# Kernel optimization log

Measured on AMD Instinct MI355X. Metric: run time of the kernel, lower is better.

The kernel has to match this reference:

```python
import jax, jax.numpy as jnp
import numpy as np

B, N, F_IN = 256, 256, 128
HID, DEPTH = 48, 4
D_OUT = 97                 # sum(latent_dim [32,32,32,1]) = GraphUNet out_channels
K_SORT = 30
C1, C2, KW2 = 16, 32, 5
POOL_LEN = (K_SORT - 2) // 2 + 1        # 15 after maxpool1d(2,2)
DENSE_DIM = (POOL_LEN - KW2 + 1) * C2   # 352
OUT_DIM = 32


def _gcn(x, A, W, b):
    # GCNConv(improved=True): A_hat = A + 2I; out = D^-1/2 A_hat D^-1/2 (x W) + b
    n = A.shape[-1]
    Ah = A + 2.0 * jnp.eye(n, dtype=A.dtype)
    dinv = jax.lax.rsqrt(jnp.sum(Ah, axis=-1))          # deg >= 2 always
    An = dinv[:, :, None] * Ah * dinv[:, None, :]
    return An @ (x @ W) + b


def _augment(A):
    # GraphUNet.augment_adj: add self loops, two-hop (A@A), remove self loops
    n = A.shape[-1]
    eye = jnp.eye(n, dtype=A.dtype)
    A1 = A + eye
    return (A1 @ A1) * (1.0 - eye)


def _topk_pool(x, A, p):
    # TopKPooling(ratio=0.5, nonlinearity=tanh): score = tanh(x.p/||p||)
    Bb, n, _ = x.shape
    score = jnp.tanh((x @ p) / jnp.sqrt(jnp.sum(p * p)))
    k = (n + 1) // 2
    vals, perm = jax.lax.top_k(score, k)                # [B,k]
    bidx = jnp.arange(Bb)[:, None]
    xp = x[bidx, perm] * vals[..., None]                # gate kept nodes by score
    Ap = A[bidx[..., None], perm[:, :, None], perm[:, None, :]]
    return xp, Ap, perm


def _forward(x, A, dW0, db0, dW, db, pool_p, uW, ub, uWl, ubl, c1W, c1b, c2W, c2b, oW, ob):
    act = jax.nn.relu
    # ---- GraphUNet down path ----
    h = act(_gcn(x, A, dW0, db0))
    xs, As, perms = [h], [A], []
    Acur = A
    for i in range(DEPTH):
        A2 = _augment(Acur)
        h, Acur, perm = _topk_pool(h, A2, pool_p[i])
        h = act(_gcn(h, Acur, dW[i], db[i]))
        if i < DEPTH - 1:
            xs.append(h)
            As.append(Acur)
        perms.append(perm)
    # ---- up path with sum skip connections ----
    for i in range(DEPTH):
        j = DEPTH - 1 - i
        res, Aj, perm = xs[j], As[j], perms[j]
        bidx = jnp.arange(res.shape[0])[:, None]
        up = jnp.zeros_like(res).at[bidx, perm].set(h)
        h = res + up
        if i < DEPTH - 1:
            h = act(_gcn(h, Aj, uW[i], ub[i]))
        else:
            h = _gcn(h, Aj, uWl, ubl)                   # [B,N,D_OUT], no act
    # ---- global_sort_pool: sort nodes by last channel desc, keep top K_SORT ----
    _, order = jax.lax.top_k(h[..., -1], K_SORT)
    sp = h[jnp.arange(B)[:, None], order]               # [B,K_SORT,D_OUT]
    # conv1d(1->C1, kernel=stride=D_OUT) on flattened [B,1,K*D] == per-node linear
    y = jax.nn.relu(jnp.einsum('bkd,cd->bck', sp, c1W) + c1b[None, :, None])  # [B,C1,K]
    y = y.reshape(B, C1, POOL_LEN, 2).max(-1)           # maxpool1d(2,2)
    y = jax.lax.conv_general_dilated(y, c2W, (1,), 'VALID',
                                     dimension_numbers=('NCH', 'OIH', 'NCH'))
    y = jax.nn.relu(y + c2b[None, :, None])             # [B,C2,POOL_LEN-KW2+1]
    return jax.nn.relu(y.reshape(B, -1) @ oW + ob)      # relu(relu(.)) == relu(.)


def setup_inputs():
    key = jax.random.key(0)
    ks = jax.random.split(key, 12)
    x = jax.random.normal(ks[0], (B, N, F_IN), dtype=jnp.float32)
    # symmetric binary adjacency, no self loops, avg degree ~15
    u = jax.random.uniform(ks[1], (B, N, N))
    A = (u < 0.03).astype(jnp.float32)
    A = jnp.maximum(A, A.transpose(0, 2, 1)) * (1.0 - jnp.eye(N, dtype=jnp.float32))
    s = lambda f: np.float32(1.0 / np.sqrt(f))
    return dict(
        x=x, A=A,
        dW0=jax.random.normal(ks[2], (F_IN, HID), dtype=jnp.float32) * s(F_IN),
        db0=jnp.zeros((HID,), jnp.float32),
        dW=jax.random.normal(ks[3], (DEPTH, HID, HID), dtype=jnp.float32) * s(HID),
        db=jnp.zeros((DEPTH, HID), jnp.float32),
        pool_p=jax.random.normal(ks[4], (DEPTH, HID), dtype=jnp.float32) * s(HID),
        uW=jax.random.normal(ks[5], (DEPTH - 1, HID, HID), dtype=jnp.float32) * s(HID),
        ub=jnp.zeros((DEPTH - 1, HID), jnp.float32),
        uWl=jax.random.normal(ks[6], (HID, D_OUT), dtype=jnp.float32) * s(HID),
        ubl=jnp.zeros((D_OUT,), jnp.float32),
        c1W=jax.random.normal(ks[7], (C1, D_OUT), dtype=jnp.float32) * s(D_OUT),
        c1b=jnp.zeros((C1,), jnp.float32),
        c2W=jax.random.normal(ks[8], (C2, C1, KW2), dtype=jnp.float32) * s(C1 * KW2),
        c2b=jnp.zeros((C2,), jnp.float32),
        oW=jax.random.normal(ks[9], (DENSE_DIM, OUT_DIM), dtype=jnp.float32) * s(DENSE_DIM),
        ob=jnp.zeros((OUT_DIM,), jnp.float32),
    )


def reference(x, A, dW0, db0, dW, db, pool_p, uW, ub, uWl, ubl, c1W, c1b, c2W, c2b, oW, ob):
    return _forward(x, A, dW0, db0, dW, db, pool_p, uW, ub, uWl, ubl, c1W, c1b, c2W, c2b, oW, ob)
```

## Files before the change

### kernel.cpp

```cpp
#include <hip/hip_runtime.h>
#include <math.h>

#define BATCH 256
#define NNODE 256
#define FIN   128
#define HID   48
#define DOUT  97

#define WOFF_DW0 0
#define WOFF_DW  6144
#define WOFF_UW  18432
#define WOFF_UWL 27648
#define WTOT     34816

typedef __attribute__((ext_vector_type(8))) short bf16x8_t;
typedef __attribute__((ext_vector_type(4))) float f32x4_t;

__device__ inline unsigned short f2bf(float x) {
  unsigned u = __float_as_uint(x);
  u += 0x7fff + ((u >> 16) & 1);
  return (unsigned short)(u >> 16);
}
__device__ inline float bf2f(unsigned short h) {
  return __uint_as_float(((unsigned)h) << 16);
}

template<int L> __device__ inline float grp_sum(float v) {
  #pragma unroll
  for (int o = L >> 1; o > 0; o >>= 1) v += __shfl_xor(v, o);
  return v;
}
template<int L> __device__ inline int grp_isum(int v) {
  #pragma unroll
  for (int o = L >> 1; o > 0; o >>= 1) v += __shfl_xor(v, o);
  return v;
}

__global__ __launch_bounds__(256) void k_splitW3(const float* __restrict__ dW0,
                                                 const float* __restrict__ dW,
                                                 const float* __restrict__ uW,
                                                 const float* __restrict__ uWl,
                                                 unsigned short* __restrict__ Wp) {
  int idx = blockIdx.x * 256 + threadIdx.x;
  if (idx >= WTOT) return;
  float v;
  if (idx < WOFF_DW) {
    int f = idx / 128, kk = idx - f * 128;
    v = dW0[kk * HID + f];
  } else if (idx < WOFF_UW) {
    int r = idx - WOFF_DW;
    int i = r / 3072; r -= i * 3072;
    int f = r / 64, kk = r - f * 64;
    v = (kk < HID) ? dW[((size_t)i * HID + kk) * HID + f] : 0.f;
  } else if (idx < WOFF_UWL) {
    int r = idx - WOFF_UW;
    int i = r / 3072; r -= i * 3072;
    int f = r / 64, kk = r - f * 64;
    v = (kk < HID) ? uW[((size_t)i * HID + kk) * HID + f] : 0.f;
  } else {
    int r = idx - WOFF_UWL;
    int f = r / 64, kk = r - f * 64;
    v = (f < DOUT && kk < HID) ? uWl[(size_t)kk * DOUT + f] : 0.f;
  }
  unsigned short h = f2bf(v);
  float r1 = v - bf2f(h);
  unsigned short m = f2bf(r1);
  float r2 = r1 - bf2f(m);
  unsigned short l = f2bf(r2);
  Wp[idx] = h;
  Wp[idx + WTOT] = m;
  Wp[idx + 2 * WTOT] = l;
}

template<int MODE>
__device__ inline void gcn128_phase(const float* __restrict__ Xg,
                                    const unsigned short* __restrict__ Wpl,
                                    const unsigned short* __restrict__ A1,
                                    const float* __restrict__ D1b,
                                    const float* __restrict__ bias,
                                    char* yt0, char* yt1,
                                    float* __restrict__ H1,
                                    float* __restrict__ H0b,
                                    const int* sPerm1, int t) {
  int w = t >> 6, lane = t & 63;
  int r = lane & 15, q = lane >> 4;
  for (int task = w; task < 24; task += 16) {
    int m = task / 3, ft = task - m * 3;
    const float* xr = Xg + (size_t)(m * 16 + r) * 48;
    bf16x8_t ah[2], am[2], al[2];
    #pragma unroll
    for (int ks = 0; ks < 2; ks++) {
      int col0 = ks * 32 + q * 8;
      float v[8];
      if (col0 + 8 <= 48) {
        float4 a4 = *(const float4*)(xr + col0);
        float4 b4 = *(const float4*)(xr + col0 + 4);
        v[0]=a4.x; v[1]=a4.y; v[2]=a4.z; v[3]=a4.w;
        v[4]=b4.x; v[5]=b4.y; v[6]=b4.z; v[7]=b4.w;
      } else {
        #pragma unroll
        for (int j = 0; j < 8; j++) v[j] = (col0 + j < 48) ? xr[col0 + j] : 0.f;
      }
      #pragma unroll
      for (int j = 0; j < 8; j++) {
        unsigned short h = f2bf(v[j]); float r1 = v[j] - bf2f(h);
        unsigned short mm = f2bf(r1);  float r2 = r1 - bf2f(mm);
        ah[ks][j] = (short)h; am[ks][j] = (short)mm; al[ks][j] = (short)f2bf(r2);
      }
    }
    int row0 = m * 16 + q * 4;
    float4 dv4 = *(const float4*)(D1b + row0);
    float dvv[4] = {dv4.x, dv4.y, dv4.z, dv4.w};
    int fl = ft * 16 + r;
    const unsigned short* wb = Wpl + (size_t)fl * 64 + q * 8;
    f32x4_t acc = {0.f, 0.f, 0.f, 0.f};
    #pragma unroll
    for (int ks = 0; ks < 2; ks++) {
      bf16x8_t bh = *(const bf16x8_t*)(wb + ks * 32);
      bf16x8_t bm = *(const bf16x8_t*)(wb + WTOT + ks * 32);
      bf16x8_t bl = *(const bf16x8_t*)(wb + 2 * WTOT + ks * 32);
      acc = __builtin_amdgcn_mfma_f32_16x16x32_bf16(ah[ks], bh, acc, 0, 0, 0);
      acc = __builtin_amdgcn_mfma_f32_16x16x32_bf16(ah[ks], bm, acc, 0, 0, 0);
      acc = __builtin_amdgcn_mfma_f32_16x16x32_bf16(am[ks], bh, acc, 0, 0, 0);
      acc = __builtin_amdgcn_mfma_f32_16x16x32_bf16(am[ks], bm, acc, 0, 0, 0);
      acc = __builtin_amdgcn_mfma_f32_16x16x32_bf16(ah[ks], bl, acc, 0, 0, 0);
      acc = __builtin_amdgcn_mfma_f32_16x16x32_bf16(al[ks], bh, acc, 0, 0, 0);
    }
    #pragma unroll
    for (int reg = 0; reg < 4; reg++) {
      float vv = dvv[reg] * acc[reg];
      unsigned short hi = f2bf(vv);
      unsigned short lo = f2bf(vv - bf2f(hi));
      int byte = (fl * 256 + (row0 + reg) * 2) ^ ((fl & 7) << 4);
      *(unsigned short*)(yt0 + byte) = hi;
      *(unsigned short*)(yt1 + byte) = lo;
    }
  }
  __syncthreads();
  for (int task = w; task < 24; task += 16) {
    int it = task / 3, ft = task - it * 3;
    const unsigned short* ap = A1 + (size_t)(it * 16 + r) * 128 + q * 8;
    bf16x8_t af[4];
    #pragma unroll
    for (int ks = 0; ks < 4; ks++) af[ks] = *(const bf16x8_t*)(ap + ks * 32);
    int fl = ft * 16 + r;
    f32x4_t acc = {0.f, 0.f, 0.f, 0.f};
    #pragma unroll
    for (int ks = 0; ks < 4; ks++) {
      int byte = (fl * 256 + (ks * 32 + q * 8) * 2) ^ ((fl & 7) << 4);
      bf16x8_t bh = *(const bf16x8_t*)(yt0 + byte);
      bf16x8_t bl = *(const bf16x8_t*)(yt1 + byte);
      acc = __builtin_amdgcn_mfma_f32_16x16x32_bf16(af[ks], bh, acc, 0, 0, 0);
      acc = __builtin_amdgcn_mfma_f32_16x16x32_bf16(af[ks], bl, acc, 0, 0, 0);
    }
    float bfv = bias[fl];
    #pragma unroll
    for (int reg = 0; reg < 4; reg++) {
      int rr = it * 16 + q * 4 + reg;
      int sbyte = (fl * 256 + rr * 2) ^ ((fl & 7) << 4);
      float selfv = bf2f(*(const unsigned short*)(yt0 + sbyte))
                  + bf2f(*(const unsigned short*)(yt1 + sbyte));
      float d = D1b[rr];
      float v = d * acc[reg] + 2.f * d * selfv + bfv;
      v = fmaxf(v, 0.f);
      if (MODE == 0) H1[(size_t)rr * 48 + fl] = v;
      else {
        int node = sPerm1[rr];
        H0b[(size_t)node * 48 + fl] += v;
      }
    }
  }
  __syncthreads();
}

__device__ inline void xw_dphase(const float* hin, const float* W, const float* dv,
                                 float* xwd, int n, int t) {
  for (int idx = t; idx < n * 48; idx += 1024) {
    int j = idx / 48, f = idx - j * 48;
    const float* hr = hin + j * 48;
    float a = 0.f;
    #pragma unroll
    for (int g = 0; g < 48; g++) a += hr[g] * W[g * 48 + f];
    xwd[idx] = dv[j] * a;
  }
}

__device__ inline void anxw_phase(const float* A, int lda, const float* xwd,
                                  const float* dv, const float* bias,
                                  float* hout, int n, int t) {
  for (int idx = t; idx < n * 48; idx += 1024) {
    int i = idx / 48, f = idx - i * 48;
    const float* ar = A + i * lda;
    float acc = 0.f;
    #pragma unroll 4
    for (int j = 0; j < n; j++) acc += ar[j] * xwd[j * 48 + f];
    float di = dv[i];
    float v = di * acc + 2.f * di * xwd[i * 48 + f] + bias[f];
    hout[idx] = fmaxf(v, 0.f);
  }
}

template<int N, int K>
__device__ inline void pool_aug_phaseT(const float* h, const float* p,
                                       const float* A, int lda,
                                       float* Ao, int ldo,
                                       float* sS, int* perm, float* hin,
                                       float* dout, int t) {
  constexpr int LPR = 1024 / N;
  int row = t / LPR, sub = t % LPR;
  float pn = 0.f;
  #pragma unroll
  for (int g = 0; g < 48; g++) pn += p[g] * p[g];
  const float* hr = h + row * 48;
  float acc = 0.f;
  for (int g = sub; g < 48; g += LPR) acc += hr[g] * p[g];
  acc = grp_sum<LPR>(acc);
  if (sub == 0) sS[row] = tanhf(acc / sqrtf(pn));
  __syncthreads();
  {
    float v = sS[row];
    int rk = 0;
    for (int j = sub; j < N; j += LPR) {
      float u = sS[j];
      rk += (u > v) || (u == v && j < row);
    }
    rk = grp_isum<LPR>(rk);
    if (sub == 0 && rk < K) perm[rk] = row;
  }
  __syncthreads();
  for (int idx = t; idx < K * 48; idx += 1024) {
    int r = idx / 48, g = idx - r * 48;
    int pi = perm[r];
    hin[idx] = h[pi * 48 + g] * sS[pi];
  }
  for (int idx = t; idx < K * K; idx += 1024) {
    int r = idx / K, c = idx - r * K;
    int pr = perm[r], pc = perm[c];
    const float* ra = A + pr * lda;
    const float* rc = A + pc * lda;
    float a2 = 0.f;
    #pragma unroll 4
    for (int j = 0; j < N; j++) a2 += ra[j] * rc[j];
    float v = a2 + 2.f * ra[pc];
    Ao[r * ldo + c] = (r == c) ? 0.f : v;
  }
  __syncthreads();
  {
    constexpr int LPR2 = 1024 / K;
    constexpr int LG = (LPR2 > 64 ? 64 : LPR2);
    int row2 = t / LPR2, sub2 = t % LPR2;
    float s = 0.f;
    for (int j = sub2; j < K; j += LPR2) s += Ao[row2 * ldo + j];
    s = grp_sum<LG>(s);
    if (sub2 == 0) dout[row2] = 1.0f / sqrtf(s + 2.0f);
  }
  __syncthreads();
}

__device__ inline void scat_phase(const int* perm, const float* src, float* dst,
                                  int k, int t) {
  for (int idx = t; idx < k * 48; idx += 1024) {
    int r = idx / 48, g = idx - r * 48;
    dst[perm[r] * 48 + g] += src[idx];
  }
  __syncthreads();
}

__global__ __launch_bounds__(1024) void k_gunet(
    const float* __restrict__ x, const float* __restrict__ A0,
    const unsigned short* __restrict__ Wp,
    const float* __restrict__ db0, const float* __restrict__ dW,
    const float* __restrict__ dbv, const float* __restrict__ pp,
    const float* __restrict__ uW, const float* __restrict__ ub,
    const float* __restrict__ ubl,
    const float* __restrict__ c1W, const float* __restrict__ c1b,
    const float* __restrict__ c2W, const float* __restrict__ c2b,
    const float* __restrict__ oW, const float* __restrict__ ob,
    unsigned short* __restrict__ Abf0g, unsigned short* __restrict__ Abf1g,
    float* __restrict__ H0g, float* __restrict__ H1g, float* __restrict__ D1g,
    float* __restrict__ out) {
  int b = blockIdx.x, t = threadIdx.x;
  __shared__ __align__(16) char arena[63488];
  __shared__ int sPerm1[128];
  __shared__ __align__(16) float sD0[256];

  const float* A0b = A0 + (size_t)b * 65536;
  unsigned short* Ab = Abf0g + (size_t)b * 65536;
  float* H0b = H0g + (size_t)b * 256 * 48;
  float* H1 = H1g + (size_t)b * 128 * 48;
  unsigned short* A1 = Abf1g + (size_t)b * 128 * 128;
  float* D1b = D1g + (size_t)b * 128;
  int w = t >> 6, lane = t & 63;
  int r = lane & 15, q = lane >> 4;

  for (int row = w; row < 256; row += 16) {
    const float4* rp = (const float4*)(A0b + (size_t)row * 256);
    float4 v = rp[lane];
    unsigned long long pk = (unsigned long long)f2bf(v.x)
                          | ((unsigned long long)f2bf(v.y) << 16)
                          | ((unsigned long long)f2bf(v.z) << 32)
                          | ((unsigned long long)f2bf(v.w) << 48);
    *(unsigned long long*)(Ab + (size_t)row * 256 + lane * 4) = pk;
    float s = v.x + v.y + v.z + v.w;
    #pragma unroll
    for (int o = 32; o > 0; o >>= 1) s += __shfl_down(s, o);
    if (lane == 0) sD0[row] = 1.0f / sqrtf(s + 2.0f);
  }
  __syncthreads();

  {
    char* yt0 = arena;
    char* yt1 = arena + 24576;
    const float* Xb = x + (size_t)b * 256 * 128;
    {
      int m = w;
      const float* xr = Xb + (size_t)(m * 16 + r) * 128;
      bf16x8_t ah[4], am[4], al[4];
      #pragma unroll
      for (int ks = 0; ks < 4; ks++) {
        int col0 = ks * 32 + q * 8;
        float4 a4 = *(const float4*)(xr + col0);
        float4 b4 = *(const float4*)(xr + col0 + 4);
        float v[8] = {a4.x, a4.y, a4.z, a4.w, b4.x, b4.y, b4.z, b4.w};
        #pragma unroll
        for (int j = 0; j < 8; j++) {
          unsigned short h = f2bf(v[j]); float r1 = v[j] - bf2f(h);
          unsigned short mm = f2bf(r1);  float r2 = r1 - bf2f(mm);
          ah[ks][j] = (short)h; am[ks][j] = (short)mm; al[ks][j] = (short)f2bf(r2);
        }
      }
      int row0 = m * 16 + q * 4;
      float4 dv4 = *(const float4*)(sD0 + row0);
      float dvv[4] = {dv4.x, dv4.y, dv4.z, dv4.w};
      #pragma unroll
      for (int ft = 0; ft < 3; ft++) {
        int fl = ft * 16 + r;
        const unsigned short* wb = Wp + WOFF_DW0 + (size_t)fl * 128 + q * 8;
        f32x4_t acc = {0.f, 0.f, 0.f, 0.f};
        #pragma unroll
        for (int ks = 0; ks < 4; ks++) {
          bf16x8_t bh = *(const bf16x8_t*)(wb + ks * 32);
          bf16x8_t bm = *(const bf16x8_t*)(wb + WTOT + ks * 32);
          bf16x8_t bl = *(const bf16x8_t*)(wb + 2 * WTOT + ks * 32);
          acc = __builtin_amdgcn_mfma_f32_16x16x32_bf16(ah[ks], bh, acc, 0, 0, 0);
          acc = __builtin_amdgcn_mfma_f32_16x16x32_bf16(ah[ks], bm, acc, 0, 0, 0);
          acc = __builtin_amdgcn_mfma_f32_16x16x32_bf16(am[ks], bh, acc, 0, 0, 0);
          acc = __builtin_amdgcn_mfma_f32_16x16x32_bf16(am[ks], bm, acc, 0, 0, 0);
          acc = __builtin_amdgcn_mfma_f32_16x16x32_bf16(ah[ks], bl, acc, 0, 0, 0);
          acc = __builtin_amdgcn_mfma_f32_16x16x32_bf16(al[ks], bh, acc, 0, 0, 0);
        }
        #pragma unroll
        for (int reg = 0; reg < 4; reg++) {
          float vv = dvv[reg] * acc[reg];
          unsigned short hi = f2bf(vv);
          unsigned short lo = f2bf(vv - bf2f(hi));
          int byte = (fl * 512 + (row0 + reg) * 2) ^ ((fl & 7) << 4);
          *(unsigned short*)(yt0 + byte) = hi;
          *(unsigned short*)(yt1 + byte) = lo;
        }
      }
    }
    __syncthreads();
    {
      int it = w;
      const unsigned short* ap = Ab + (size_t)(it * 16 + r) * 256 + q * 8;
      bf16x8_t af[8];
      #pragma unroll
      for (int ks = 0; ks < 8; ks++) af[ks] = *(const bf16x8_t*)(ap + ks * 32);
      #pragma unroll
      for (int ft = 0; ft < 3; ft++) {
        int fl = ft * 16 + r;
        f32x4_t acc = {0.f, 0.f, 0.f, 0.f};
        #pragma unroll
        for (int ks = 0; ks < 8; ks++) {
          int byte = (fl * 512 + (ks * 32 + q * 8) * 2) ^ ((fl & 7) << 4);
          bf16x8_t bh = *(const bf16x8_t*)(yt0 + byte);
          bf16x8_t bl = *(const bf16x8_t*)(yt1 + byte);
          acc = __builtin_amdgcn_mfma_f32_16x16x32_bf16(af[ks], bh, acc, 0, 0, 0);
          acc = __builtin_amdgcn_mfma_f32_16x16x32_bf16(af[ks], bl, acc, 0, 0, 0);
        }
        float bfv = db0[fl];
        #pragma unroll
        for (int reg = 0; reg < 4; reg++) {
          int rr = it * 16 + q * 4 + reg;
          int sbyte = (fl * 512 + rr * 2) ^ ((fl & 7) << 4);
          float selfv = bf2f(*(const unsigned short*)(yt0 + sbyte))
                      + bf2f(*(const unsigned short*)(yt1 + sbyte));
          float d = sD0[rr];
          float v = d * acc[reg] + 2.f * d * selfv + bfv;
          H0b[(size_t)rr * 48 + fl] = fmaxf(v, 0.f);
        }
      }
    }
  }
  __syncthreads();

  {
    float* sc = (float*)arena;
    const float* p = pp;
    float pn = 0.f;
    #pragma unroll
    for (int g = 0; g < 48; g++) pn += p[g] * p[g];
    int row = t >> 2, sub = t & 3;
    const float* hr = H0b + (size_t)row * 48;
    float a = 0.f;
    for (int g = sub; g < 48; g += 4) a += hr[g] * p[g];
    a = grp_sum<4>(a);
    if (!sub) sc[row] = tanhf(a / sqrtf(pn));
    __syncthreads();
    float vv = sc[row];
    int rk = 0;
    for (int j = sub; j < 256; j += 4) {
      float u = sc[j];
      rk += (u > vv) || (u == vv && j < row);
    }
    rk = grp_isum<4>(rk);
    if (!sub && rk < 128) sPerm1[rk] = row;
  }
  __syncthreads();

  {
    float* sc = (float*)arena;
    for (int idx = t; idx < 128 * 48; idx += 1024) {
      int rr = idx / 48, g = idx - rr * 48;
      int pi = sPerm1[rr];
      H1[idx] = H0b[(size_t)pi * 48 + g] * sc[pi];
    }
    int it = w >> 1, fh = w & 1;
    int rowA = sPerm1[it * 16 + r];
    const unsigned short* pa = Ab + (size_t)rowA * 256 + q * 8;
    bf16x8_t af[8];
    #pragma unroll
    for (int ks = 0; ks < 8; ks++) {
      bf16x8_t a = *(const bf16x8_t*)(pa + ks * 32);
      int da = rowA - ks * 32 - q * 8;
      #pragma unroll
      for (int e = 0; e < 8; e++) if (da == e) a[e] = (short)0x3F80;
      af[ks] = a;
    }
    for (int ft = fh * 4; ft < fh * 4 + 4; ft++) {
      int rowB = sPerm1[ft * 16 + r];
      const unsigned short* pb = Ab + (size_t)rowB * 256 + q * 8;
      f32x4_t acc = {0.f, 0.f, 0.f, 0.f};
      #pragma unroll
      for (int ks = 0; ks < 8; ks++) {
        bf16x8_t bv = *(const bf16x8_t*)(pb + ks * 32);
        int db_ = rowB - ks * 32 - q * 8;
        #pragma unroll
        for (int e = 0; e < 8; e++) if (db_ == e) bv[e] = (short)0x3F80;
        acc = __builtin_amdgcn_mfma_f32_16x16x32_bf16(af[ks], bv, acc, 0, 0, 0);
      }
      int c = ft * 16 + r;
      #pragma unroll
      for (int reg = 0; reg < 4; reg++) {
        int rr = it * 16 + q * 4 + reg;
        float v = (rr == c) ? 0.f : acc[reg];
        A1[(size_t)rr * 128 + c] = f2bf(v);
      }
    }
  }
  __syncthreads();
  {
    int row = t >> 3, sub = t & 7;
    const unsigned* ar = (const unsigned*)(A1 + (size_t)row * 128);
    float s = 0.f;
    for (int jj = sub; jj < 64; jj += 8) {
      unsigned u = ar[jj];
      s += bf2f((unsigned short)(u & 0xffffu)) + bf2f((unsigned short)(u >> 16));
    }
    s = grp_sum<8>(s);
    if (sub == 0) D1b[row] = 1.0f / sqrtf(s + 2.0f);
  }
  __syncthreads();

  gcn128_phase<0>(H1, Wp + WOFF_DW, A1, D1b, dbv,
                  arena, arena + 12288, H1, nullptr, sPerm1, t);

  {
    float* sS  = (float*)(arena);
    int*   sP2 = (int*)(arena + 512);
    int*   sP3 = (int*)(arena + 768);
    int*   sP4 = (int*)(arena + 896);
    float* sD2 = (float*)(arena + 960);
    float* sD3 = (float*)(arena + 1216);
    float* sD4 = (float*)(arena + 1344);
    float* sA2 = (float*)(arena + 1536);
    float* sA3 = (float*)(arena + 18176);
    float* sH2 = (float*)(arena + 22400);
    float* sH3 = (float*)(arena + 34688);
    float* sXW = (float*)(arena + 40832);
    float* hin = (float*)(arena + 53120);
    float* sH4 = (float*)(arena + 59264);
    float* sA4 = (float*)(arena + 62336);

    {
      const float* p = pp + 48;
      float pn = 0.f;
      #pragma unroll
      for (int g = 0; g < 48; g++) pn += p[g] * p[g];
      int row = t >> 3, sub = t & 7;
      const float* hr = H1 + (size_t)row * 48;
      float acc = 0.f;
      for (int g = sub; g < 48; g += 8) acc += hr[g] * p[g];
      acc = grp_sum<8>(acc);
      if (sub == 0) sS[row] = tanhf(acc / sqrtf(pn));
      __syncthreads();
      float v = sS[row];
      int rk = 0;
      for (int j = sub; j < 128; j += 8) {
        float u = sS[j];
        rk += (u > v) || (u == v && j < row);
      }
      rk = grp_isum<8>(rk);
      if (sub == 0 && rk < 64) sP2[rk] = row;
      __syncthreads();
    }
    {
      int it = w >> 2, ft = w & 3;
      int rowA = sP2[it * 16 + r];
      int rowB = sP2[ft * 16 + r];
      const unsigned short* pa = A1 + (size_t)rowA * 128 + q * 8;
      const unsigned short* pb = A1 + (size_t)rowB * 128 + q * 8;
      f32x4_t acc = {0.f, 0.f, 0.f, 0.f};
      #pragma unroll
      for (int k0 = 0; k0 < 128; k0 += 32) {
        bf16x8_t a  = *(const bf16x8_t*)(pa + k0);
        bf16x8_t bv = *(const bf16x8_t*)(pb + k0);
        int daA = rowA - k0 - q * 8;
        int daB = rowB - k0 - q * 8;
        #pragma unroll
        for (int e = 0; e < 8; e++) {
          if (daA == e) a[e] = (short)0x3F80;
          if (daB == e) bv[e] = (short)0x3F80;
        }
        acc = __builtin_amdgcn_mfma_f32_16x16x32_bf16(a, bv, acc, 0, 0, 0);
      }
      int c = ft * 16 + r;
      #pragma unroll
      for (int reg = 0; reg < 4; reg++) {
        int rr = it * 16 + q * 4 + reg;
        sA2[rr * 65 + c] = (rr == c) ? 0.f : acc[reg];
      }
    }
    __syncthreads();
    {
      int row = t >> 4, sub = t & 15;
      float s = 0.f;
      for (int j = sub; j < 64; j += 16) s += sA2[row * 65 + j];
      s = grp_sum<16>(s);
      if (sub == 0) sD2[row] = 1.0f / sqrtf(s + 2.0f);
    }
    __syncthreads();
    for (int idx = t; idx < 64 * 48; idx += 1024) {
      int j = idx / 48, f = idx - j * 48;
      int pi = sP2[j];
      const float* hr = H1 + (size_t)pi * 48;
      const float* W = dW + 2304;
      float a = 0.f;
      #pragma unroll
      for (int g = 0; g < 48; g++) a += hr[g] * W[g * 48 + f];
      sXW[idx] = sD2[j] * sS[pi] * a;
    }
    __syncthreads();
    anxw_phase(sA2, 65, sXW, sD2, dbv + 48, sH2, 64, t);
    __syncthreads();

    pool_aug_phaseT<64, 32>(sH2, pp + 96, sA2, 65, sA3, 33, sS, sP3, hin, sD3, t);
    xw_dphase(hin, dW + 2 * 2304, sD3, sXW, 32, t);
    __syncthreads();
    anxw_phase(sA3, 33, sXW, sD3, dbv + 96, sH3, 32, t);
    __syncthreads();

    pool_aug_phaseT<32, 16>(sH3, pp + 144, sA3, 33, sA4, 17, sS, sP4, hin, sD4, t);
    xw_dphase(hin, dW + 3 * 2304, sD4, sXW, 16, t);
    __syncthreads();
    anxw_phase(sA4, 17, sXW, sD4, dbv + 144, sH4, 16, t);
    __syncthreads();

    scat_phase(sP4, sH4, sH3, 16, t);
    xw_dphase(sH3, uW, sD3, sXW, 32, t);
    __syncthreads();
    anxw_phase(sA3, 33, sXW, sD3, ub, sH3, 32, t);
    __syncthreads();

    scat_phase(sP3, sH3, sH2, 32, t);
    xw_dphase(sH2, uW + 2304, sD2, sXW, 64, t);
    __syncthreads();
    anxw_phase(sA2, 65, sXW, sD2, ub + 48, sH2, 64, t);
    __syncthreads();

    for (int idx = t; idx < 64 * 48; idx += 1024) {
      int r2 = idx / 48, g = idx - r2 * 48;
      H1[(size_t)sP2[r2] * 48 + g] += sH2[idx];
    }
  }
  __syncthreads();

  gcn128_phase<1>(H1, Wp + WOFF_UW + 2 * 3072, A1, D1b, ub + 96,
                  arena, arena + 12288, nullptr, H0b, sPerm1, t);

  float* spl = (float*)(arena + 16448);
  {
    float* ydt = (float*)arena;
    float* scp = (float*)(arena + 28096);
    int* sord  = (int*)(arena + 29120);

    bf16x8_t ah[2], am[2], al[2];
    {
      const float* xr = H0b + (size_t)(w * 16 + r) * 48;
      #pragma unroll
      for (int ks = 0; ks < 2; ks++) {
        int col0 = ks * 32 + q * 8;
        float v[8];
        if (col0 + 8 <= 48) {
          float4 a4 = *(const float4*)(xr + col0);
          float4 b4 = *(const float4*)(xr + col0 + 4);
          v[0]=a4.x; v[1]=a4.y; v[2]=a4.z; v[3]=a4.w;
          v[4]=b4.x; v[5]=b4.y; v[6]=b4.z; v[7]=b4.w;
        } else {
          #pragma unroll
          for (int j = 0; j < 8; j++) v[j] = (col0 + j < 48) ? xr[col0 + j] : 0.f;
        }
        #pragma unroll
        for (int j = 0; j < 8; j++) {
          unsigned short h = f2bf(v[j]); float r1 = v[j] - bf2f(h);
          unsigned short mm = f2bf(r1);  float r2 = r1 - bf2f(mm);
          ah[ks][j] = (short)h; am[ks][j] = (short)mm; al[ks][j] = (short)f2bf(r2);
        }
      }
    }
    int row0 = w * 16 + q * 4;
    float4 dv4 = *(const float4*)(sD0 + row0);
    float dvv[4] = {dv4.x, dv4.y, dv4.z, dv4.w};

    auto stepA = [&](int ft) {
      int fl = ft * 16 + r;
      const unsigned short* wb = Wp + WOFF_UWL + (size_t)fl * 64 + q * 8;
      f32x4_t acc = {0.f, 0.f, 0.f, 0.f};
      #pragma unroll
      for (int ks = 0; ks < 2; ks++) {
        bf16x8_t bh = *(const bf16x8_t*)(wb + ks * 32);
        bf16x8_t bm = *(const bf16x8_t*)(wb + WTOT + ks * 32);
        bf16x8_t bl = *(const bf16x8_t*)(wb + 2 * WTOT + ks * 32);
        acc = __builtin_amdgcn_mfma_f32_16x16x32_bf16(ah[ks], bh, acc, 0, 0, 0);
        acc = __builtin_amdgcn_mfma_f32_16x16x32_bf16(ah[ks], bm, acc, 0, 0, 0);
        acc = __builtin_amdgcn_mfma_f32_16x16x32_bf16(am[ks], bh, acc, 0, 0, 0);
        acc = __builtin_amdgcn_mfma_f32_16x16x32_bf16(am[ks], bm, acc, 0, 0, 0);
        acc = __builtin_amdgcn_mfma_f32_16x16x32_bf16(ah[ks], bl, acc, 0, 0, 0);
        acc = __builtin_amdgcn_mfma_f32_16x16x32_bf16(al[ks], bh, acc, 0, 0, 0);
      }
      #pragma unroll
      for (int reg = 0; reg < 4; reg++)
        ydt[r * 257 + row0 + reg] = dvv[reg] * acc[reg];
    };

    auto stepB = [&](int ft, int nf) {
      int o = t >> 1, sub = t & 1;
      if (o < 30 * nf) {
        int rr = o / nf, f = o - rr * nf;
        int fl = ft * 16 + f;
        int node = sord[rr];
        const unsigned short* ar = Ab + (size_t)node * 256 + sub * 128;
        const float* yp = &ydt[f * 257 + sub * 128];
        float s = 0.f;
        for (int j = 0; j < 128; j += 2) {
          unsigned u = *(const unsigned*)(ar + j);
          s += bf2f((unsigned short)(u & 0xffffu)) * yp[j]
             + bf2f((unsigned short)(u >> 16)) * yp[j + 1];
        }
        s += __shfl_xor(s, 1);
        if (!sub) {
          float d = sD0[node];
          spl[rr * DOUT + fl] = d * s + 2.f * d * ydt[f * 257 + node] + ubl[fl];
        }
      }
    };

    stepA(6);
    __syncthreads();
    {
      int i = t >> 2, sub = t & 3;
      const unsigned short* ar = Ab + (size_t)i * 256 + sub * 64;
      const float* yp = &ydt[0 * 257 + sub * 64];
      float s = 0.f;
      for (int j = 0; j < 64; j += 2) {
        unsigned u = *(const unsigned*)(ar + j);
        s += bf2f((unsigned short)(u & 0xffffu)) * yp[j]
           + bf2f((unsigned short)(u >> 16)) * yp[j + 1];
      }
      s = grp_sum<4>(s);
      if (!sub) {
        float d = sD0[i];
        scp[i] = d * s + 2.f * d * ydt[0 * 257 + i];
      }
    }
    __syncthreads();
    {
      int i = t >> 2, sub = t & 3;
      float v = scp[i];
      int rk = 0;
      int j0 = sub * 64;
      for (int j = j0; j < j0 + 64; j++) {
        float u = scp[j];
        rk += (u > v) || (u == v && j < i);
      }
      rk = grp_isum<4>(rk);
      if (!sub && rk < 30) sord[rk] = i;
    }
    __syncthreads();
    stepB(6, 1);
    __syncthreads();
    for (int ft = 0; ft < 6; ft++) {
      stepA(ft);
      __syncthreads();
      stepB(ft, 16);
      __syncthreads();
    }
  }

  {
    float* y1  = (float*)(arena + 32768);
    float* yp  = (float*)(arena + 34688);
    float* yc  = (float*)(arena + 35648);
    float* red = (float*)(arena + 37056);
    for (int idx = t; idx < 16 * 30; idx += 1024) {
      int c = idx / 30, kk = idx - c * 30;
      float a = c1b[c];
      for (int d = 0; d < 97; d++) a += spl[kk * 97 + d] * c1W[c * 97 + d];
      y1[c * 30 + kk] = fmaxf(a, 0.f);
    }
    __syncthreads();
    for (int idx = t; idx < 16 * 15; idx += 1024) {
      int c = idx / 15, t2 = idx - c * 15;
      yp[idx] = fmaxf(y1[c * 30 + 2 * t2], y1[c * 30 + 2 * t2 + 1]);
    }
    __syncthreads();
    for (int idx = t; idx < 32 * 11; idx += 1024) {
      int o = idx / 11, t3 = idx - o * 11;
      float a = c2b[o];
      for (int i2 = 0; i2 < 16; i2++)
        for (int ww = 0; ww < 5; ww++)
          a += yp[i2 * 15 + t3 + ww] * c2W[(o * 16 + i2) * 5 + ww];
      yc[o * 11 + t3] = fmaxf(a, 0.f);
    }
    __syncthreads();
    {
      int o = t & 31, g = t >> 5;
      float a = 0.f;
      for (int qq = g * 11; qq < g * 11 + 11; qq++) a += yc[qq] * oW[qq * 32 + o];
      red[t] = a;
    }
    __syncthreads();
    if (t < 32) {
      float a = ob[t];
      #pragma unroll
      for (int g = 0; g < 32; g++) a += red[t + 32 * g];
      out[(size_t)b * 32 + t] = fmaxf(a, 0.f);
    }
  }
}

extern "C" void kernel_launch(void* const* d_in, const int* in_sizes, int n_in,
                              void* d_out, int out_size, void* d_ws, size_t ws_size,
                              hipStream_t stream) {
  const float* x   = (const float*)d_in[0];
  const float* A0  = (const float*)d_in[1];
  const float* dW0 = (const float*)d_in[2];
  const float* db0 = (const float*)d_in[3];
  const float* dW  = (const float*)d_in[4];
  const float* dbv = (const float*)d_in[5];
  const float* pp  = (const float*)d_in[6];
  const float* uW  = (const float*)d_in[7];
  const float* ub  = (const float*)d_in[8];
  const float* uWl = (const float*)d_in[9];
  const float* ubl = (const float*)d_in[10];
  const float* c1W = (const float*)d_in[11];
  const float* c1b = (const float*)d_in[12];
  const float* c2W = (const float*)d_in[13];
  const float* c2b = (const float*)d_in[14];
  const float* oW  = (const float*)d_in[15];
  const float* ob  = (const float*)d_in[16];
  float* out = (float*)d_out;

  float* base = (float*)d_ws;
  size_t off = 0;
  auto alloc = [&](size_t nel) { nel = (nel + 3) & ~(size_t)3; float* p = base + off; off += nel; return p; };
  float* H0 = alloc((size_t)BATCH * 256 * HID);
  float* H1 = alloc((size_t)BATCH * 128 * HID);
  float* D1 = alloc((size_t)BATCH * 128);
  unsigned short* Abf0 = (unsigned short*)alloc((size_t)BATCH * 256 * 256 / 2);
  unsigned short* Abf1 = (unsigned short*)alloc((size_t)BATCH * 128 * 128 / 2);
  unsigned short* Wp   = (unsigned short*)alloc((size_t)3 * WTOT / 2 + 4);

  k_splitW3<<<(WTOT + 255) / 256, 256, 0, stream>>>(dW0, dW, uW, uWl, Wp);

  k_gunet<<<BATCH, 1024, 0, stream>>>(x, A0, Wp, db0, dW, dbv, pp, uW, ub, ubl,
                                      c1W, c1b, c2W, c2b, oW, ob,
                                      Abf0, Abf1, H0, H1, D1, out);
}
```

Measured before the change: 377.8 us.

## Double-buffer final GCN stage, stage sorted A rows in LDS, fuse degree prologue

```diff
diff --git a/kernel.cpp b/kernel.cpp
--- a/kernel.cpp
+++ b/kernel.cpp
@@ -293,21 +293,25 @@
   int w = t >> 6, lane = t & 63;
   int r = lane & 15, q = lane >> 4;
 
-  for (int row = w; row < 256; row += 16) {
-    const float4* rp = (const float4*)(A0b + (size_t)row * 256);
-    float4 v = rp[lane];
-    unsigned long long pk = (unsigned long long)f2bf(v.x)
-                          | ((unsigned long long)f2bf(v.y) << 16)
-                          | ((unsigned long long)f2bf(v.z) << 32)
-                          | ((unsigned long long)f2bf(v.w) << 48);
-    *(unsigned long long*)(Ab + (size_t)row * 256 + lane * 4) = pk;
-    float s = v.x + v.y + v.z + v.w;
-    #pragma unroll
-    for (int o = 32; o > 0; o >>= 1) s += __shfl_down(s, o);
-    if (lane == 0) sD0[row] = 1.0f / sqrtf(s + 2.0f);
-  }
-  __syncthreads();
-
+  float dvv0[4];
+  {
+    #pragma unroll
+    for (int i = 0; i < 16; i++) {
+      int row = w * 16 + i;
+      const float4* rp = (const float4*)(A0b + (size_t)row * 256);
+      float4 v = rp[lane];
+      unsigned long long pk = (unsigned long long)f2bf(v.x)
+                            | ((unsigned long long)f2bf(v.y) << 16)
+                            | ((unsigned long long)f2bf(v.z) << 32)
+                            | ((unsigned long long)f2bf(v.w) << 48);
+      *(unsigned long long*)(Ab + (size_t)row * 256 + lane * 4) = pk;
+      float s = v.x + v.y + v.z + v.w;
+      s = grp_sum<64>(s);
+      float dval = 1.0f / sqrtf(s + 2.0f);
+      if (lane == 0) sD0[row] = dval;
+      if (q == (i >> 2)) dvv0[i & 3] = dval;
+    }
+  }
   {
     char* yt0 = arena;
     char* yt1 = arena + 24576;
@@ -330,8 +334,6 @@
         }
       }
       int row0 = m * 16 + q * 4;
-      float4 dv4 = *(const float4*)(sD0 + row0);
-      float dvv[4] = {dv4.x, dv4.y, dv4.z, dv4.w};
       #pragma unroll
       for (int ft = 0; ft < 3; ft++) {
         int fl = ft * 16 + r;
@@ -351,7 +353,7 @@
         }
         #pragma unroll
         for (int reg = 0; reg < 4; reg++) {
-          float vv = dvv[reg] * acc[reg];
+          float vv = dvv0[reg] * acc[reg];
           unsigned short hi = f2bf(vv);
           unsigned short lo = f2bf(vv - bf2f(hi));
           int byte = (fl * 512 + (row0 + reg) * 2) ^ ((fl & 7) << 4);
@@ -599,11 +601,13 @@
   gcn128_phase<1>(H1, Wp + WOFF_UW + 2 * 3072, A1, D1b, ub + 96,
                   arena, arena + 12288, nullptr, H0b, sPerm1, t);
 
-  float* spl = (float*)(arena + 16448);
-  {
-    float* ydt = (float*)arena;
-    float* scp = (float*)(arena + 28096);
-    int* sord  = (int*)(arena + 29120);
+  float* spl = (float*)(arena + 32896);
+  {
+    float* ydA = (float*)arena;
+    float* ydB = (float*)(arena + 16448);
+    unsigned* sAr = (unsigned*)(arena + 44536);
+    float* scp = (float*)(arena + 60496);
+    int* sord  = (int*)(arena + 61520);
 
     bf16x8_t ah[2], am[2], al[2];
     {
@@ -633,7 +637,7 @@
     float4 dv4 = *(const float4*)(sD0 + row0);
     float dvv[4] = {dv4.x, dv4.y, dv4.z, dv4.w};
 
-    auto stepA = [&](int ft) {
+    auto stepA = [&](int ft, float* ydt) {
       int fl = ft * 16 + r;
       const unsigned short* wb = Wp + WOFF_UWL + (size_t)fl * 64 + q * 8;
       f32x4_t acc = {0.f, 0.f, 0.f, 0.f};
@@ -654,19 +658,20 @@
         ydt[r * 257 + row0 + reg] = dvv[reg] * acc[reg];
     };
 
-    auto stepB = [&](int ft, int nf) {
+    auto stepB = [&](int ft, int nf, const float* ydt) {
       int o = t >> 1, sub = t & 1;
       if (o < 30 * nf) {
         int rr = o / nf, f = o - rr * nf;
         int fl = ft * 16 + f;
         int node = sord[rr];
-        const unsigned short* ar = Ab + (size_t)node * 256 + sub * 128;
+        const unsigned* ar = sAr + rr * 133 + sub * 64;
         const float* yp = &ydt[f * 257 + sub * 128];
         float s = 0.f;
-        for (int j = 0; j < 128; j += 2) {
-          unsigned u = *(const unsigned*)(ar + j);
-          s += bf2f((unsigned short)(u & 0xffffu)) * yp[j]
-             + bf2f((unsigned short)(u >> 16)) * yp[j + 1];
+        #pragma unroll 4
+        for (int j = 0; j < 64; j++) {
+          unsigned u = ar[j];
+          s += bf2f((unsigned short)(u & 0xffffu)) * yp[2 * j]
+             + bf2f((unsigned short)(u >> 16)) * yp[2 * j + 1];
         }
         s += __shfl_xor(s, 1);
         if (!sub) {
@@ -676,12 +681,12 @@
       }
     };
 
-    stepA(6);
+    stepA(6, ydA);
     __syncthreads();
     {
       int i = t >> 2, sub = t & 3;
       const unsigned short* ar = Ab + (size_t)i * 256 + sub * 64;
-      const float* yp = &ydt[0 * 257 + sub * 64];
+      const float* yp = &ydA[0 * 257 + sub * 64];
       float s = 0.f;
       for (int j = 0; j < 64; j += 2) {
         unsigned u = *(const unsigned*)(ar + j);
@@ -691,7 +696,7 @@
       s = grp_sum<4>(s);
       if (!sub) {
         float d = sD0[i];
-        scp[i] = d * s + 2.f * d * ydt[0 * 257 + i];
+        scp[i] = d * s + 2.f * d * ydA[0 * 257 + i];
       }
     }
     __syncthreads();
@@ -708,21 +713,26 @@
       if (!sub && rk < 30) sord[rk] = i;
     }
     __syncthreads();
-    stepB(6, 1);
-    __syncthreads();
-    for (int ft = 0; ft < 6; ft++) {
-      stepA(ft);
-      __syncthreads();
-      stepB(ft, 16);
-      __syncthreads();
-    }
-  }
-
-  {
-    float* y1  = (float*)(arena + 32768);
-    float* yp  = (float*)(arena + 34688);
-    float* yc  = (float*)(arena + 35648);
-    float* red = (float*)(arena + 37056);
+    for (int idx = t; idx < 30 * 128; idx += 1024) {
+      int rr = idx >> 7, cc = idx & 127;
+      sAr[rr * 133 + cc] = ((const unsigned*)(Ab + (size_t)sord[rr] * 256))[cc];
+    }
+    __syncthreads();
+    stepA(0, ydB); stepB(6, 1, ydA);  __syncthreads();
+    stepA(1, ydA); stepB(0, 16, ydB); __syncthreads();
+    stepA(2, ydB); stepB(1, 16, ydA); __syncthreads();
+    stepA(3, ydA); stepB(2, 16, ydB); __syncthreads();
+    stepA(4, ydB); stepB(3, 16, ydA); __syncthreads();
+    stepA(5, ydA); stepB(4, 16, ydB); __syncthreads();
+    stepB(5, 16, ydA);
+    __syncthreads();
+  }
+
+  {
+    float* y1  = (float*)(arena);
+    float* yp  = (float*)(arena + 2048);
+    float* yc  = (float*)(arena + 3072);
+    float* red = (float*)(arena + 4608);
     for (int idx = t; idx < 16 * 30; idx += 1024) {
       int c = idx / 30, kk = idx - c * 30;
       float a = c1b[c];
```

Result: no change. 380.1 us (+0.6%).
